# Optimization experiments

Hardware: AMD Instinct MI355X
Metric: run time of the kernel (lower is better)

Reference implementation:

```python
import jax, jax.numpy as jnp
import numpy as np

B, L, DIM = 2, 2048, 1024
H, DH, W = 16, 64, 256  # heads, head_dim, window_size
ROPE_BASE = 10000.0


def _rope(x):
    # x: [b, l, h, d] -> rotate consecutive pairs (torch view_as_complex semantics)
    l, d = x.shape[1], x.shape[3]
    freqs = 1.0 / (ROPE_BASE ** (jnp.arange(0, d, 2, dtype=jnp.float32) / d))  # [d/2]
    ang = jnp.arange(l, dtype=jnp.float32)[:, None] * freqs[None, :]           # [l, d/2]
    cos = jnp.cos(ang)[None, :, None, :].astype(x.dtype)
    sin = jnp.sin(ang)[None, :, None, :].astype(x.dtype)
    xe, xo = x[..., 0::2], x[..., 1::2]
    ye = xe * cos - xo * sin
    yo = xe * sin + xo * cos
    return jnp.stack([ye, yo], axis=-1).reshape(x.shape)


def setup_inputs() -> dict:
    key = jax.random.key(0)
    ks = jax.random.split(key, 7)
    sh = (B, L, DIM)
    return {
        "q": jax.random.normal(ks[0], sh, jnp.float32),
        "k": jax.random.normal(ks[1], sh, jnp.float32),
        "v": jax.random.normal(ks[2], sh, jnp.float32),
        "wq": jax.random.normal(ks[3], (H * DH, DIM), jnp.float32) * 0.02,
        "wk": jax.random.normal(ks[4], (H * DH, DIM), jnp.float32) * 0.02,
        "wv": jax.random.normal(ks[5], (H * DH, DIM), jnp.float32) * 0.02,
        "wo": jax.random.normal(ks[6], (DIM, H * DH), jnp.float32) * 0.02,
    }


def reference(q, k, v, wq, wk, wv, wo):
    b, l, _ = q.shape
    qh = (q @ wq.T).reshape(b, l, H, DH)
    kh = (k @ wk.T).reshape(b, l, H, DH)
    vh = (v @ wv.T).reshape(b, l, H, DH).transpose(0, 2, 1, 3)  # [b,h,l,d]
    qh = _rope(qh).transpose(0, 2, 1, 3)                        # [b,h,l,d]
    kh = _rope(kh).transpose(0, 2, 1, 3)
    scores = jnp.einsum('bhqd,bhkd->bhqk', qh, kh) * (DH ** -0.5)
    i = jnp.arange(l)[:, None]
    j = jnp.arange(l)[None, :]
    window_mask = (j <= i) & (j >= i - W)  # keys in [i-W, i], matches the loop
    scores = jnp.where(window_mask, scores, -1e30)
    probs = jax.nn.softmax(scores, axis=-1)
    out = jnp.einsum('bhqk,bhkd->bhqd', probs, vh)
    out = out.transpose(0, 2, 1, 3).reshape(b, l, H * DH)
    return out @ wo.T
```

## Files before the change

kernel.cpp:

```cpp
#include <hip/hip_runtime.h>
#include <stdint.h>

#define B_    2
#define L_    2048
#define DIM_  1024
#define H_    16
#define DH_   64
#define WWIN  256

typedef __attribute__((ext_vector_type(4))) float f32x4;
typedef __attribute__((ext_vector_type(8))) short bf16x8;

__device__ __forceinline__ unsigned short f2bf(float x) {
  union { float f; unsigned u; } c; c.f = x;
  unsigned r = c.u + 0x7fffu + ((c.u >> 16) & 1u);
  return (unsigned short)(r >> 16);
}

struct CastArgs {
  const float* src[7];
  unsigned short* dst[7];
};
__global__ __launch_bounds__(256) void cast_bf16_kernel(CastArgs a) {
  int bid = blockIdx.x;
  int arr, base;
  if (bid < 12288) {
    arr = bid >> 12;
    base = (bid & 4095) << 10;
  } else {
    int t = bid - 12288;
    arr = 3 + (t >> 10);
    base = (t & 1023) << 10;
  }
  int i = base + (int)threadIdx.x * 4;
  float4 v = *(const float4*)(a.src[arr] + i);
  ushort4 o;
  o.x = f2bf(v.x); o.y = f2bf(v.y); o.z = f2bf(v.z); o.w = f2bf(v.w);
  *(ushort4*)(a.dst[arr] + i) = o;
}

#define BM 128
#define BN 64
#define BK 64

__device__ __forceinline__ void gld_lds16(const void* g, void* l) {
  __builtin_amdgcn_global_load_lds(
      (const __attribute__((address_space(1))) void*)g,
      (__attribute__((address_space(3))) void*)l, 16, 0, 0);
}

__device__ __forceinline__ void gemm_core_1024(
    const unsigned short* __restrict__ A, const unsigned short* __restrict__ Bt,
    unsigned short* As, unsigned short* Bs, f32x4 (&acc)[2][4],
    int m0, int n0) {
  const int tid = threadIdx.x;
  const int wave = tid >> 6, lane = tid & 63;
  const int quad = lane >> 4, l16 = lane & 15;
  const int srow = tid >> 3, sc = tid & 7;

  auto stage = [&](int k0, int buf) {
    unsigned short* Ad = As + buf * 8192;
    unsigned short* Bd = Bs + buf * 4096;
    #pragma unroll
    for (int rd = 0; rd < 4; ++rd) {
      int row = rd * 32 + srow;
      int cs = sc ^ (row & 7);
      gld_lds16(A + (size_t)(m0 + row) * 1024 + k0 + cs * 8, Ad + row * BK + sc * 8);
    }
    #pragma unroll
    for (int rd = 0; rd < 2; ++rd) {
      int row = rd * 32 + srow;
      int cs = sc ^ (row & 7);
      gld_lds16(Bt + (size_t)(n0 + row) * 1024 + k0 + cs * 8, Bd + row * BK + sc * 8);
    }
  };

  stage(0, 0);
  for (int k = 0; k < 16; ++k) {
    const int cur = k & 1;
    __syncthreads();
    if (k < 15) stage((k + 1) * BK, cur ^ 1);
    const unsigned short* Ac = As + cur * 8192;
    const unsigned short* Bc = Bs + cur * 4096;
    #pragma unroll
    for (int ks = 0; ks < 2; ++ks) {
      bf16x8 af[2], bfr[4];
      #pragma unroll
      for (int i = 0; i < 2; ++i) {
        int row = wave * 32 + i * 16 + l16;
        int ch = (ks * 4 + quad) ^ (row & 7);
        af[i] = *(const bf16x8*)(Ac + row * BK + ch * 8);
      }
      #pragma unroll
      for (int j = 0; j < 4; ++j) {
        int row = j * 16 + l16;
        int ch = (ks * 4 + quad) ^ (row & 7);
        bfr[j] = *(const bf16x8*)(Bc + row * BK + ch * 8);
      }
      #pragma unroll
      for (int i = 0; i < 2; ++i)
        #pragma unroll
        for (int j = 0; j < 4; ++j)
          acc[i][j] = __builtin_amdgcn_mfma_f32_16x16x32_bf16(af[i], bfr[j], acc[i][j], 0, 0, 0);
    }
  }
}

struct ProjArgs {
  const unsigned short* A[3];
  const unsigned short* Bt[3];
  unsigned short* C[3];
};
__global__ __launch_bounds__(256) void gemm_proj_kernel(ProjArgs pa) {
  __shared__ unsigned short SH[24576];
  unsigned short* As = SH;
  unsigned short* Bs = SH + 16384;

  const int bflat = blockIdx.x;
  const int xcd = bflat & 7, s = bflat >> 3;
  const int nblk = s & 15;
  const int mz = xcd * 12 + (s >> 4);
  const int z = mz >> 5;
  const int mblk = mz & 31;
  const int m0 = mblk * BM, n0 = nblk * BN;

  f32x4 acc[2][4] = {};
  gemm_core_1024(pa.A[z], pa.Bt[z], As, Bs, acc, m0, n0);

  const int tid = threadIdx.x;
  const int lane = tid & 63, wave = tid >> 6;
  const int quad = lane >> 4, l16 = lane & 15;

  if (z < 2) {
    float frev[4];
    #pragma unroll
    for (int j = 0; j < 4; ++j) {
      int d = j * 16 + l16;
      frev[j] = exp2f(-(float)(d >> 1) * 0.41524101186092029f) * 0.15915494309189535f;
    }
    unsigned short* C = pa.C[z];
    const int h = nblk;
    const bool even = (l16 & 1) == 0;
    #pragma unroll
    for (int i = 0; i < 2; ++i)
      #pragma unroll
      for (int r = 0; r < 4; ++r) {
        int m = m0 + wave * 32 + i * 16 + quad * 4 + r;
        int b = m >> 11, l = m & (L_ - 1);
        float lf = (float)l;
        #pragma unroll
        for (int j = 0; j < 4; ++j) {
          int d = j * 16 + l16;
          float v = acc[i][j][r];
          float p = __shfl_xor(v, 1);
          float a = lf * frev[j];
          float t = a - floorf(a);
          float sn = __builtin_amdgcn_sinf(t);
          float cs = __builtin_amdgcn_cosf(t);
          float o = even ? (v * cs - p * sn) : (p * sn + v * cs);
          C[(((size_t)b * H_ + h) * L_ + l) * DH_ + d] = f2bf(o);
        }
      }
  } else {
    __syncthreads();
    unsigned short* T = SH + wave * 2304;
    #pragma unroll
    for (int i = 0; i < 2; ++i)
      #pragma unroll
      for (int j = 0; j < 4; ++j) {
        int nw = j * 16 + l16;
        int hm = i * 4 + quad;
        uint2 pk;
        pk.x = (unsigned)f2bf(acc[i][j][0]) | ((unsigned)f2bf(acc[i][j][1]) << 16);
        pk.y = (unsigned)f2bf(acc[i][j][2]) | ((unsigned)f2bf(acc[i][j][3]) << 16);
        *(uint2*)(T + nw * 36 + hm * 4) = pk;
      }
    asm volatile("s_waitcnt lgkmcnt(0)" ::: "memory");
    int h = nblk;
    int d = lane;
    int b = m0 >> 11;
    int lbase = (m0 & (L_ - 1)) + wave * 32;
    unsigned short* C = pa.C[2];
    size_t rowbase = (((size_t)b * H_ + h) * DH_ + d) * L_ + lbase;
    #pragma unroll
    for (int t = 0; t < 4; ++t) {
      uint2 lo = *(uint2*)(T + lane * 36 + t * 8);
      uint2 hi = *(uint2*)(T + lane * 36 + t * 8 + 4);
      uint4 o = {lo.x, lo.y, hi.x, hi.y};
      *(uint4*)(C + rowbase + t * 8) = o;
    }
  }
}

__global__ __launch_bounds__(256) void gemm_out_kernel(
    const unsigned short* __restrict__ A, const unsigned short* __restrict__ Bt,
    float* __restrict__ C) {
  __shared__ unsigned short SH[24576];
  unsigned short* As = SH;
  unsigned short* Bs = SH + 16384;

  const int bflat = blockIdx.x;
  const int xcd = bflat & 7, s = bflat >> 3;
  const int nblk = s & 15;
  const int mblk = xcd * 4 + (s >> 4);
  const int m0 = mblk * BM, n0 = nblk * BN;

  f32x4 acc[2][4] = {};
  gemm_core_1024(A, Bt, As, Bs, acc, m0, n0);

  const int lane = threadIdx.x & 63, wave = threadIdx.x >> 6;
  const int quad = lane >> 4, l16 = lane & 15;
  #pragma unroll
  for (int i = 0; i < 2; ++i)
    #pragma unroll
    for (int j = 0; j < 4; ++j)
      #pragma unroll
      for (int r = 0; r < 4; ++r) {
        int m = m0 + wave * 32 + i * 16 + quad * 4 + r;
        int n = n0 + j * 16 + l16;
        C[(size_t)m * DIM_ + n] = acc[i][j][r];
      }
}

#define NCH 20
__global__ __launch_bounds__(256) void attn_kernel(
    const unsigned short* __restrict__ Qh,
    const unsigned short* __restrict__ Kh,
    const unsigned short* __restrict__ Vt,
    unsigned short* __restrict__ O) {
  __shared__ unsigned short KVs[64 * 168];
  __shared__ unsigned short Ps[4][16 * 172];
  const int tid = threadIdx.x;
  const int wave = tid >> 6, lane = tid & 63;
  const int quad = lane >> 4, l16 = lane & 15;

  const int bflat = blockIdx.x;
  const int xcd = bflat & 7, s = bflat >> 3;
  const int qt = s >> 2;
  const int bh = xcd * 4 + (s & 3);

  const int q0 = qt * 64;
  const int kwin0 = q0 - WWIN;
  const int qb = q0 + wave * 16;
  const bool edge = (kwin0 < 0);

  bf16x8 qf0, qf1;
  {
    const unsigned short* qrow = Qh + ((size_t)bh * L_ + qb + l16) * DH_;
    qf0 = *(const bf16x8*)(qrow + quad * 8);
    qf1 = *(const bf16x8*)(qrow + 32 + quad * 8);
  }

  f32x4 S[NCH] = {};

  const int srow = tid >> 3, sc = tid & 7;
  #pragma unroll
  for (int half = 0; half < 2; ++half) {
    __syncthreads();
    #pragma unroll
    for (int rep = 0; rep < 5; ++rep) {
      int row = rep * 32 + srow;
      int key = kwin0 + half * 160 + row;
      key = key < 0 ? 0 : key;
      int cs = sc ^ (row & 7);
      gld_lds16(Kh + ((size_t)bh * L_ + key) * DH_ + cs * 8,
                (unsigned short*)KVs + row * 64 + sc * 8);
    }
    __syncthreads();
    #pragma unroll
    for (int cc = 0; cc < 10; ++cc) {
      const int c = half * 10 + cc;
      if (c < wave || c > wave + 16) continue;
      int row = cc * 16 + l16;
      const unsigned short* kr = (const unsigned short*)KVs + row * 64;
      bf16x8 kf0 = *(const bf16x8*)(kr + ((quad) ^ (row & 7)) * 8);
      bf16x8 kf1 = *(const bf16x8*)(kr + ((4 + quad) ^ (row & 7)) * 8);
      S[c] = __builtin_amdgcn_mfma_f32_16x16x32_bf16(qf0, kf0, S[c], 0, 0, 0);
      S[c] = __builtin_amdgcn_mfma_f32_16x16x32_bf16(qf1, kf1, S[c], 0, 0, 0);
    }
  }

  float inv_l[4];
  #pragma unroll
  for (int r = 0; r < 4; ++r) {
    const int i = qb + quad * 4 + r;
    float mx = -1e30f;
    #pragma unroll
    for (int c = 0; c < NCH; ++c) {
      if (c < wave || c > wave + 16) continue;
      float v = S[c][r];
      if (edge || c == wave || c == wave + 16) {
        int key = kwin0 + c * 16 + l16;
        bool valid = (key >= 0) && (key <= i) && (key >= i - WWIN);
        v = valid ? v : -1e30f;
        S[c][r] = v;
      }
      mx = fmaxf(mx, v);
    }
    mx = fmaxf(mx, __shfl_xor(mx, 1));
    mx = fmaxf(mx, __shfl_xor(mx, 2));
    mx = fmaxf(mx, __shfl_xor(mx, 4));
    mx = fmaxf(mx, __shfl_xor(mx, 8));
    float sum = 0.f;
    #pragma unroll
    for (int c = 0; c < NCH; ++c) {
      if (c < wave || c > wave + 16) continue;
      float e = __builtin_amdgcn_exp2f((S[c][r] - mx) * 0.18033688011112042f);
      S[c][r] = e;
      sum += e;
    }
    sum += __shfl_xor(sum, 1);
    sum += __shfl_xor(sum, 2);
    sum += __shfl_xor(sum, 4);
    sum += __shfl_xor(sum, 8);
    inv_l[r] = 1.0f / sum;
  }

  f32x4 Oacc[4] = {};
  unsigned short* pw = &Ps[wave][0];
  #pragma unroll
  for (int half = 0; half < 2; ++half) {
    const int glo = (half == 0) ? (wave >> 1) : 0;
    const int ghi = (half == 0) ? 4 : ((wave + 6) >> 1);
    __syncthreads();
    for (int rep = 0; rep < 5; ++rep) {
      int ci = rep * 256 + tid;
      int row = ci / 20, c = ci % 20;
      int key0 = kwin0 + half * 160 + c * 8;
      uint4 val = {0, 0, 0, 0};
      if (key0 >= 0)
        val = *(const uint4*)(Vt + ((size_t)bh * DH_ + row) * L_ + key0);
      *(uint4*)(&KVs[row * 168 + c * 8]) = val;
    }
    #pragma unroll
    for (int cc = 0; cc < 10; ++cc) {
      if ((cc >> 1) < glo || (cc >> 1) > ghi) continue;
      #pragma unroll
      for (int r = 0; r < 4; ++r) {
        float p = S[half * 10 + cc][r] * inv_l[r];
        pw[(quad * 4 + r) * 172 + cc * 16 + l16] = f2bf(p);
      }
    }
    __syncthreads();
    #pragma unroll
    for (int s5 = 0; s5 < 5; ++s5) {
      if (s5 < glo || s5 > ghi) continue;
      bf16x8 pf = *(const bf16x8*)(pw + l16 * 172 + s5 * 32 + quad * 8);
      int lk = s5 * 32 + quad * 8;
      #pragma unroll
      for (int t = 0; t < 4; ++t) {
        bf16x8 vf = *(const bf16x8*)(&KVs[(t * 16 + l16) * 168 + lk]);
        Oacc[t] = __builtin_amdgcn_mfma_f32_16x16x32_bf16(pf, vf, Oacc[t], 0, 0, 0);
      }
    }
  }

  int b = bh >> 4, h = bh & 15;
  #pragma unroll
  for (int t = 0; t < 4; ++t)
    #pragma unroll
    for (int r = 0; r < 4; ++r) {
      int l = qb + quad * 4 + r;
      int col = h * DH_ + t * 16 + l16;
      O[((size_t)b * L_ + l) * (H_ * DH_) + col] = f2bf(Oacc[t][r]);
    }
}

extern "C" void kernel_launch(void* const* d_in, const int* in_sizes, int n_in,
                              void* d_out, int out_size, void* d_ws, size_t ws_size,
                              hipStream_t stream) {
  const float* q  = (const float*)d_in[0];
  const float* k  = (const float*)d_in[1];
  const float* v  = (const float*)d_in[2];
  const float* wq = (const float*)d_in[3];
  const float* wk = (const float*)d_in[4];
  const float* wv = (const float*)d_in[5];
  const float* wo = (const float*)d_in[6];

  const size_t SA = (size_t)B_ * L_ * DIM_;
  const size_t SW = (size_t)DIM_ * DIM_;
  unsigned short* w   = (unsigned short*)d_ws;
  unsigned short* qb  = w; w += SA;
  unsigned short* kb  = w; w += SA;
  unsigned short* vb  = w; w += SA;
  unsigned short* wqb = w; w += SW;
  unsigned short* wkb = w; w += SW;
  unsigned short* wvb = w; w += SW;
  unsigned short* wob = w; w += SW;
  unsigned short* qh  = w; w += SA;
  unsigned short* kh  = w; w += SA;
  unsigned short* vt  = w; w += SA;
  unsigned short* Ob  = w; w += SA;

  CastArgs ca;
  ca.src[0] = q;  ca.dst[0] = qb;
  ca.src[1] = k;  ca.dst[1] = kb;
  ca.src[2] = v;  ca.dst[2] = vb;
  ca.src[3] = wq; ca.dst[3] = wqb;
  ca.src[4] = wk; ca.dst[4] = wkb;
  ca.src[5] = wv; ca.dst[5] = wvb;
  ca.src[6] = wo; ca.dst[6] = wob;
  cast_bf16_kernel<<<dim3(16384), 256, 0, stream>>>(ca);

  ProjArgs pa;
  pa.A[0] = qb; pa.Bt[0] = wqb; pa.C[0] = qh;
  pa.A[1] = kb; pa.Bt[1] = wkb; pa.C[1] = kh;
  pa.A[2] = vb; pa.Bt[2] = wvb; pa.C[2] = vt;
  gemm_proj_kernel<<<dim3(16 * 32 * 3), 256, 0, stream>>>(pa);

  attn_kernel<<<dim3(32 * 32), 256, 0, stream>>>(qh, kh, vt, Ob);
  gemm_out_kernel<<<dim3(16 * 32), 256, 0, stream>>>(Ob, wob, (float*)d_out);
}
```

Measured before the change: 189.8 us.

## Enlarge projection GEMM tile to 128x128 with single-buffered LDS

Switches the QKV projection GEMM from 128x64 tiles to 128x128 tiles, with each wave computing a 64x64 sub-tile and covering two heads, which halves the grid to 768 blocks. The goal is more data reuse per LDS load and fewer blocks re-reading A. The new core drops the double-buffered prefetch and syncs twice per k-step, so load latency is no longer hidden. The V-transpose epilogue is rewritten to use an XOR-swizzled LDS staging buffer.

```diff
diff --git a/kernel.cpp b/kernel.cpp
--- a/kernel.cpp
+++ b/kernel.cpp
@@ -49,6 +49,56 @@
       (__attribute__((address_space(3))) void*)l, 16, 0, 0);
 }
 
+__device__ __forceinline__ void gemm_core_128x128(
+    const unsigned short* __restrict__ A, const unsigned short* __restrict__ Bt,
+    unsigned short* As, unsigned short* Bs, f32x4 (&acc)[4][4],
+    int m0, int n0) {
+  const int tid = threadIdx.x;
+  const int wave = tid >> 6, lane = tid & 63;
+  const int quad = lane >> 4, l16 = lane & 15;
+  const int wm = wave >> 1, wn = wave & 1;
+  const int srow = tid >> 3, sc = tid & 7;
+
+  for (int k = 0; k < 16; ++k) {
+    const int k0 = k * 64;
+    #pragma unroll
+    for (int rd = 0; rd < 4; ++rd) {
+      int row = rd * 32 + srow;
+      int cs = sc ^ (row & 7);
+      gld_lds16(A + (size_t)(m0 + row) * 1024 + k0 + cs * 8, As + row * 64 + sc * 8);
+    }
+    #pragma unroll
+    for (int rd = 0; rd < 4; ++rd) {
+      int row = rd * 32 + srow;
+      int cs = sc ^ (row & 7);
+      gld_lds16(Bt + (size_t)(n0 + row) * 1024 + k0 + cs * 8, Bs + row * 64 + sc * 8);
+    }
+    __syncthreads();
+    #pragma unroll
+    for (int ks = 0; ks < 2; ++ks) {
+      bf16x8 af[4], bfr[4];
+      #pragma unroll
+      for (int i = 0; i < 4; ++i) {
+        int row = wm * 64 + i * 16 + l16;
+        int ch = (ks * 4 + quad) ^ (row & 7);
+        af[i] = *(const bf16x8*)(As + row * 64 + ch * 8);
+      }
+      #pragma unroll
+      for (int j = 0; j < 4; ++j) {
+        int row = wn * 64 + j * 16 + l16;
+        int ch = (ks * 4 + quad) ^ (row & 7);
+        bfr[j] = *(const bf16x8*)(Bs + row * 64 + ch * 8);
+      }
+      #pragma unroll
+      for (int i = 0; i < 4; ++i)
+        #pragma unroll
+        for (int j = 0; j < 4; ++j)
+          acc[i][j] = __builtin_amdgcn_mfma_f32_16x16x32_bf16(af[i], bfr[j], acc[i][j], 0, 0, 0);
+    }
+    __syncthreads();
+  }
+}
+
 __device__ __forceinline__ void gemm_core_1024(
     const unsigned short* __restrict__ A, const unsigned short* __restrict__ Bt,
     unsigned short* As, unsigned short* Bs, f32x4 (&acc)[2][4],
@@ -112,24 +162,26 @@
   unsigned short* C[3];
 };
 __global__ __launch_bounds__(256) void gemm_proj_kernel(ProjArgs pa) {
-  __shared__ unsigned short SH[24576];
+  __shared__ unsigned short SH[16384];
   unsigned short* As = SH;
-  unsigned short* Bs = SH + 16384;
+  unsigned short* Bs = SH + 8192;
 
   const int bflat = blockIdx.x;
   const int xcd = bflat & 7, s = bflat >> 3;
-  const int nblk = s & 15;
-  const int mz = xcd * 12 + (s >> 4);
+  const int nblk = s & 7;
+  const int mz = xcd * 12 + (s >> 3);
   const int z = mz >> 5;
   const int mblk = mz & 31;
-  const int m0 = mblk * BM, n0 = nblk * BN;
-
-  f32x4 acc[2][4] = {};
-  gemm_core_1024(pa.A[z], pa.Bt[z], As, Bs, acc, m0, n0);
+  const int m0 = mblk * BM, n0 = nblk * 128;
+
+  f32x4 acc[4][4] = {};
+  gemm_core_128x128(pa.A[z], pa.Bt[z], As, Bs, acc, m0, n0);
 
   const int tid = threadIdx.x;
   const int lane = tid & 63, wave = tid >> 6;
   const int quad = lane >> 4, l16 = lane & 15;
+  const int wm = wave >> 1, wn = wave & 1;
+  const int h = nblk * 2 + wn;
 
   if (z < 2) {
     float frev[4];
@@ -139,13 +191,12 @@
       frev[j] = exp2f(-(float)(d >> 1) * 0.41524101186092029f) * 0.15915494309189535f;
     }
     unsigned short* C = pa.C[z];
-    const int h = nblk;
     const bool even = (l16 & 1) == 0;
     #pragma unroll
-    for (int i = 0; i < 2; ++i)
+    for (int i = 0; i < 4; ++i)
       #pragma unroll
       for (int r = 0; r < 4; ++r) {
-        int m = m0 + wave * 32 + i * 16 + quad * 4 + r;
+        int m = m0 + wm * 64 + i * 16 + quad * 4 + r;
         int b = m >> 11, l = m & (L_ - 1);
         float lf = (float)l;
         #pragma unroll
@@ -162,32 +213,29 @@
         }
       }
   } else {
-    __syncthreads();
-    unsigned short* T = SH + wave * 2304;
-    #pragma unroll
-    for (int i = 0; i < 2; ++i)
+    char* T = (char*)SH + wave * 8192;
+    #pragma unroll
+    for (int i = 0; i < 4; ++i)
       #pragma unroll
       for (int j = 0; j < 4; ++j) {
-        int nw = j * 16 + l16;
-        int hm = i * 4 + quad;
+        int d = j * 16 + l16;
+        int mb = i * 32 + quad * 8;
+        int ch = mb >> 4, sub = mb & 15;
         uint2 pk;
         pk.x = (unsigned)f2bf(acc[i][j][0]) | ((unsigned)f2bf(acc[i][j][1]) << 16);
         pk.y = (unsigned)f2bf(acc[i][j][2]) | ((unsigned)f2bf(acc[i][j][3]) << 16);
-        *(uint2*)(T + nw * 36 + hm * 4) = pk;
+        *(uint2*)(T + d * 128 + ((ch ^ (d & 7)) << 4) + sub) = pk;
       }
     asm volatile("s_waitcnt lgkmcnt(0)" ::: "memory");
-    int h = nblk;
-    int d = lane;
     int b = m0 >> 11;
-    int lbase = (m0 & (L_ - 1)) + wave * 32;
+    int lbase = (m0 & (L_ - 1)) + wm * 64;
     unsigned short* C = pa.C[2];
-    size_t rowbase = (((size_t)b * H_ + h) * DH_ + d) * L_ + lbase;
-    #pragma unroll
-    for (int t = 0; t < 4; ++t) {
-      uint2 lo = *(uint2*)(T + lane * 36 + t * 8);
-      uint2 hi = *(uint2*)(T + lane * 36 + t * 8 + 4);
-      uint4 o = {lo.x, lo.y, hi.x, hi.y};
-      *(uint4*)(C + rowbase + t * 8) = o;
+    #pragma unroll
+    for (int t = 0; t < 8; ++t) {
+      int d = t * 8 + (lane >> 3);
+      int ch = lane & 7;
+      uint4 o = *(uint4*)(T + d * 128 + ((ch ^ (d & 7)) << 4));
+      *(uint4*)(C + (((size_t)b * H_ + h) * DH_ + d) * L_ + lbase + ch * 8) = o;
     }
   }
 }
@@ -406,7 +454,7 @@
   pa.A[0] = qb; pa.Bt[0] = wqb; pa.C[0] = qh;
   pa.A[1] = kb; pa.Bt[1] = wkb; pa.C[1] = kh;
   pa.A[2] = vb; pa.Bt[2] = wvb; pa.C[2] = vt;
-  gemm_proj_kernel<<<dim3(16 * 32 * 3), 256, 0, stream>>>(pa);
+  gemm_proj_kernel<<<dim3(768), 256, 0, stream>>>(pa);
 
   attn_kernel<<<dim3(32 * 32), 256, 0, stream>>>(qh, kh, vt, Ob);
   gemm_out_kernel<<<dim3(16 * 32), 256, 0, stream>>>(Ob, wob, (float*)d_out);
```

Result: slower. 199.7 us (+5.2%).
